# Performance work log

Measured on AMD Instinct MI355X. Metric: run time of the kernel, lower is better.

Reference implementation:

```python
import jax, jax.numpy as jnp
import numpy as np

B, Q, C, NH, NL, NP, DFF = 8, 300, 256, 8, 4, 4, 1024
DH = C // NH
SHAPES = [(100, 100), (50, 50), (25, 25), (13, 13)]  # (H, W) per level
LEN = sum(h * w for h, w in SHAPES)


def _ln(x, g, b):
    m = x.mean(-1, keepdims=True)
    v = ((x - m) ** 2).mean(-1, keepdims=True)
    return (x - m) / jnp.sqrt(v + 1e-5) * g + b


def _bilinear(v, loc, H, W):
    # v: [B, NH, H*W, DH]; loc: [B, NH, Q, NP, 2] normalized to [0,1]
    # grid_sample(align_corners=False, padding_mode='zeros') semantics
    x = loc[..., 0] * W - 0.5
    y = loc[..., 1] * H - 0.5
    x0 = jnp.floor(x)
    y0 = jnp.floor(y)
    dx = x - x0
    dy = y - y0
    out = jnp.zeros(x.shape + (v.shape[-1],), v.dtype)
    for xi, yi, wgt in ((x0, y0, (1 - dx) * (1 - dy)),
                        (x0 + 1, y0, dx * (1 - dy)),
                        (x0, y0 + 1, (1 - dx) * dy),
                        (x0 + 1, y0 + 1, dx * dy)):
        valid = ((xi >= 0) & (xi < W) & (yi >= 0) & (yi < H)).astype(v.dtype)
        idx = jnp.clip(yi, 0, H - 1).astype(jnp.int32) * W + jnp.clip(xi, 0, W - 1).astype(jnp.int32)
        g = jnp.take_along_axis(v, idx.reshape(idx.shape[0], idx.shape[1], -1)[..., None], axis=2)
        out = out + (wgt * valid)[..., None] * g.reshape(x.shape + (v.shape[-1],))
    return out


def _forward(tgt, reference_points, memory, query_pos_embed,
             Wq, bq, Wk, bk, Wv, bv, Wo, bo, g1, be1,
             W_off, b_off, W_attn, b_attn, W_val, b_val, W_out, b_out, g2, be2,
             W1, b1, W2, b2, g3, be3):
    scale = 1.0 / float(np.sqrt(DH))
    # ---- self attention (q = k = tgt + pos, v = tgt) ----
    qk = tgt + query_pos_embed
    q = (qk @ Wq + bq).reshape(B, Q, NH, DH)
    k = (qk @ Wk + bk).reshape(B, Q, NH, DH)
    v = (tgt @ Wv + bv).reshape(B, Q, NH, DH)
    attn = jax.nn.softmax(jnp.einsum('bqhd,bkhd->bhqk', q, k) * scale, axis=-1)
    sa = jnp.einsum('bhqk,bkhd->bqhd', attn, v).reshape(B, Q, C) @ Wo + bo
    t = _ln(tgt + sa, g1, be1)
    # ---- multi-scale deformable cross attention ----
    query = t + query_pos_embed
    value = (memory @ W_val + b_val).reshape(B, LEN, NH, DH).transpose(0, 2, 1, 3)  # [B,NH,LEN,DH]
    off = (query @ W_off + b_off).reshape(B, Q, NH, NL, NP, 2)
    aw = jax.nn.softmax((query @ W_attn + b_attn).reshape(B, Q, NH, NL * NP), axis=-1)
    aw = aw.reshape(B, Q, NH, NL, NP)
    wh = jnp.array([[w, h] for h, w in SHAPES], jnp.float32)  # offset normalizer (W, H)
    loc = reference_points[:, :, None, :, None, :] + off / wh[None, None, None, :, None, :]
    out = jnp.zeros((B, NH, Q, DH), t.dtype)
    start = 0
    for l, (h, w) in enumerate(SHAPES):
        v_l = value[:, :, start:start + h * w]
        loc_l = loc[:, :, :, l].transpose(0, 2, 1, 3, 4)  # [B,NH,Q,NP,2]
        samp = _bilinear(v_l, loc_l, h, w)                # [B,NH,Q,NP,DH]
        out = out + (samp * aw[:, :, :, l].transpose(0, 2, 1, 3)[..., None]).sum(3)
        start += h * w
    ca = out.transpose(0, 2, 1, 3).reshape(B, Q, C) @ W_out + b_out
    t = _ln(t + ca, g2, be2)
    # ---- FFN ----
    ff = jax.nn.relu(t @ W1 + b1) @ W2 + b2
    return _ln(t + ff, g3, be3)


def setup_inputs() -> dict:
    ks = jax.random.split(jax.random.key(0), 16)
    z, o = jnp.zeros, jnp.ones
    w = lambda i, sh: jax.random.normal(ks[i], sh, jnp.float32) * 0.02
    return {
        'tgt': jax.random.normal(ks[0], (B, Q, C), jnp.float32),
        'reference_points': jax.random.uniform(ks[1], (B, Q, NL, 2), jnp.float32),
        'memory': jax.random.normal(ks[2], (B, LEN, C), jnp.float32),
        'query_pos_embed': jax.random.normal(ks[3], (B, Q, C), jnp.float32),
        'Wq': w(4, (C, C)), 'bq': z(C), 'Wk': w(5, (C, C)), 'bk': z(C),
        'Wv': w(6, (C, C)), 'bv': z(C), 'Wo': w(7, (C, C)), 'bo': z(C),
        'g1': o(C), 'be1': z(C),
        'W_off': w(8, (C, NH * NL * NP * 2)), 'b_off': z(NH * NL * NP * 2),
        'W_attn': w(9, (C, NH * NL * NP)), 'b_attn': z(NH * NL * NP),
        'W_val': w(10, (C, C)), 'b_val': z(C), 'W_out': w(11, (C, C)), 'b_out': z(C),
        'g2': o(C), 'be2': z(C),
        'W1': w(12, (C, DFF)), 'b1': z(DFF), 'W2': w(13, (DFF, C)), 'b2': z(C),
        'g3': o(C), 'be3': z(C),
        'spatial_shapes': jnp.array(SHAPES, jnp.int32),
        'level_start_index': jnp.array(np.cumsum([0] + [h * w for h, w in SHAPES[:-1]]), jnp.int32),
    }


def reference(tgt, reference_points, memory, query_pos_embed,
              Wq, bq, Wk, bk, Wv, bv, Wo, bo, g1, be1,
              W_off, b_off, W_attn, b_attn, W_val, b_val, W_out, b_out, g2, be2,
              W1, b1, W2, b2, g3, be3, spatial_shapes, level_start_index):
    return _forward(tgt, reference_points, memory, query_pos_embed,
                    Wq, bq, Wk, bk, Wv, bv, Wo, bo, g1, be1,
                    W_off, b_off, W_attn, b_attn, W_val, b_val, W_out, b_out, g2, be2,
                    W1, b1, W2, b2, g3, be3)
```

## Files before the change

### kernel.cpp

```cpp
#include <hip/hip_runtime.h>
#include <hip/hip_bf16.h>
#include <math.h>

#define B_   8
#define Q_   300
#define C_   256
#define NH_  8
#define NL_  4
#define NP_  4
#define DFF_ 1024
#define DH_  32
#define LEN_ 13294
#define MQ_  (B_*Q_)
#define MV_  (B_*LEN_)
#define NSTRIP_ 3324

typedef __attribute__((ext_vector_type(4))) float f32x4;
typedef __attribute__((ext_vector_type(8))) short bf16x8;
typedef __hip_bfloat16 bf16;

#define GLOAD16(gp, lp) __builtin_amdgcn_global_load_lds( \
    (const __attribute__((address_space(1))) unsigned int*)(gp), \
    (__attribute__((address_space(3))) unsigned int*)(lp), 16, 0, 0)

__device__ __forceinline__ short f2bfbits(float x) {
    bf16 h = __float2bfloat16(x);
    return *reinterpret_cast<short*>(&h);
}


__device__ __forceinline__ void gmm64_body(char* smemraw, int bx, int by,
        const bf16* __restrict__ A, const bf16* __restrict__ Bt,
        const float* __restrict__ bias0, const float* __restrict__ bias1, int nsplit,
        float* __restrict__ outf, bf16* __restrict__ outh,
        int M, int N, int K, int RELU, int OUT_MODE) {
    bf16* As = (bf16*)smemraw;
    bf16* Bs = (bf16*)(smemraw + 4096);
    const int tid  = threadIdx.x;
    const int wid  = tid >> 6, lane = tid & 63;
    const int m0 = by * 64, n0 = bx * 64;
    const int wr = wid >> 1, wc = wid & 1;
    const int fr = lane & 15, fq = lane >> 4;
    const int rloc = wid * 16 + (lane >> 2);
    const int kof  = (lane & 3) * 8;
    f32x4 acc[2][2] = {};
    for (int k0 = 0; k0 < K; k0 += 32) {
        if (k0) __syncthreads();
        int gr = m0 + rloc; if (gr > M - 1) gr = M - 1;
        GLOAD16(A + (size_t)gr * K + k0 + kof, As + rloc * 32);
        int gc = n0 + rloc; if (gc > N - 1) gc = N - 1;
        GLOAD16(Bt + (size_t)gc * K + k0 + kof, Bs + rloc * 32);
        __syncthreads();
        bf16x8 af[2], bfr[2];
#pragma unroll
        for (int m = 0; m < 2; ++m)
            af[m] = *(const bf16x8*)(As + (wr * 32 + m * 16 + fr) * 32 + fq * 8);
#pragma unroll
        for (int n = 0; n < 2; ++n)
            bfr[n] = *(const bf16x8*)(Bs + (wc * 32 + n * 16 + fr) * 32 + fq * 8);
#pragma unroll
        for (int m = 0; m < 2; ++m)
#pragma unroll
            for (int n = 0; n < 2; ++n)
                acc[m][n] = __builtin_amdgcn_mfma_f32_16x16x32_bf16(af[m], bfr[n], acc[m][n], 0, 0, 0);
    }
#pragma unroll
    for (int m = 0; m < 2; ++m) {
#pragma unroll
        for (int n = 0; n < 2; ++n) {
            const int c = n0 + wc * 32 + n * 16 + fr;
            const float bs = (c < nsplit) ? bias0[c] : bias1[c - nsplit];
#pragma unroll
            for (int j = 0; j < 4; ++j) {
                const int r = m0 + wr * 32 + m * 16 + fq * 4 + j;
                if (r >= M) continue;
                float v = acc[m][n][j] + bs;
                if (RELU) v = fmaxf(v, 0.f);
                if (OUT_MODE == 0) outf[(size_t)r * N + c] = v;
                else               outh[(size_t)r * N + c] = __float2bfloat16(v);
            }
        }
    }
}

__device__ __forceinline__ void gmmV_body(char* smemraw, int bid,
        const float* __restrict__ A, const bf16* __restrict__ Bt,
        const float* __restrict__ bias, bf16* __restrict__ outh, int M) {
    short (*As)[8192] = (short(*)[8192])smemraw;
    const int tid = threadIdx.x;
    const int w = tid >> 6, lane = tid & 63;
    const int fr = lane & 15, fq = lane >> 4;
    const int r   = tid >> 3;
    const int itc = tid & 7;

    bf16x8 bc[4][8];
#pragma unroll
    for (int n = 0; n < 4; ++n)
#pragma unroll
        for (int it = 0; it < 8; ++it)
            bc[n][it] = *(const bf16x8*)(Bt + (size_t)(w * 64 + n * 16 + fr) * 256 + it * 32 + fq * 8);
    float bs[4];
#pragma unroll
    for (int n = 0; n < 4; ++n) bs[n] = bias[w * 64 + n * 16 + fr];

    const int sbase = bid * 4;
    float4 pf[8];

#define LOADA(s_) { \
        int row_ = (s_) * 32 + r; if (row_ > M - 1) row_ = M - 1; \
        const float4* p_ = (const float4*)(A + (size_t)row_ * 256 + itc * 32); \
        pf[0] = p_[0]; pf[1] = p_[1]; pf[2] = p_[2]; pf[3] = p_[3]; \
        pf[4] = p_[4]; pf[5] = p_[5]; pf[6] = p_[6]; pf[7] = p_[7]; }
#define WRITEA(buf_) { \
        short* dst_ = &As[buf_][itc * 1024 + r * 32]; \
        _Pragma("unroll") \
        for (int g_ = 0; g_ < 4; ++g_) { \
            float4 a0_ = pf[2 * g_], a1_ = pf[2 * g_ + 1]; \
            union { short h[8]; bf16x8 v; } cv_; \
            cv_.h[0] = f2bfbits(a0_.x); cv_.h[1] = f2bfbits(a0_.y); \
            cv_.h[2] = f2bfbits(a0_.z); cv_.h[3] = f2bfbits(a0_.w); \
            cv_.h[4] = f2bfbits(a1_.x); cv_.h[5] = f2bfbits(a1_.y); \
            cv_.h[6] = f2bfbits(a1_.z); cv_.h[7] = f2bfbits(a1_.w); \
            *(bf16x8*)(dst_ + g_ * 8) = cv_.v; \
        } }

    LOADA(sbase);
    WRITEA(0);
    __syncthreads();
    int buf = 0;
#pragma unroll 1
    for (int i = 0; i < 4; ++i) {
        const int s = sbase + i;
        if (s >= NSTRIP_) break;
        const bool more = (i < 3) && (s + 1 < NSTRIP_);
        if (more) LOADA(s + 1);
        f32x4 acc[2][4] = {};
#pragma unroll
        for (int it = 0; it < 8; ++it) {
            bf16x8 af[2];
#pragma unroll
            for (int m = 0; m < 2; ++m)
                af[m] = *(const bf16x8*)&As[buf][it * 1024 + (m * 16 + fr) * 32 + fq * 8];
#pragma unroll
            for (int m = 0; m < 2; ++m)
#pragma unroll
                for (int n = 0; n < 4; ++n)
                    acc[m][n] = __builtin_amdgcn_mfma_f32_16x16x32_bf16(af[m], bc[n][it], acc[m][n], 0, 0, 0);
        }
        if (more) WRITEA(buf ^ 1);
#pragma unroll
        for (int m = 0; m < 2; ++m)
#pragma unroll
            for (int n = 0; n < 4; ++n) {
                const int c = w * 64 + n * 16 + fr;
#pragma unroll
                for (int j = 0; j < 4; ++j) {
                    const int row = s * 32 + m * 16 + fq * 4 + j;
                    if (row < M)
                        outh[(size_t)row * 256 + c] = __float2bfloat16(acc[m][n][j] + bs[n]);
                }
            }
        if (more) __syncthreads();
        buf ^= 1;
    }
#undef LOADA
#undef WRITEA
}


__global__ __launch_bounds__(256) void k_prep(
        const float* __restrict__ Wq, const float* __restrict__ Wk,
        const float* __restrict__ Wv, const float* __restrict__ Wo,
        const float* __restrict__ Wval, const float* __restrict__ Woff,
        const float* __restrict__ Wattn, const float* __restrict__ Wout,
        const float* __restrict__ W1, const float* __restrict__ W2,
        bf16* __restrict__ Wqk_t, bf16* __restrict__ Wv_t, bf16* __restrict__ Wo_t,
        bf16* __restrict__ Wval_t, bf16* __restrict__ Woa_t, bf16* __restrict__ Wout_t,
        bf16* __restrict__ W1_t, bf16* __restrict__ W2_t,
        const float* __restrict__ tgt, const float* __restrict__ qpe,
        bf16* __restrict__ qk_o, bf16* __restrict__ tgt_o) {
    __shared__ float t[32][33];
    const int id = blockIdx.x;
    if (id < 992) {
        const float* W; bf16* D; int K, N, r;
        if      (id < 64)  { W = Wq;    D = Wqk_t;          K = 256;  N = 256;  r = id; }
        else if (id < 128) { W = Wk;    D = Wqk_t + 65536;  K = 256;  N = 256;  r = id - 64; }
        else if (id < 192) { W = Wv;    D = Wv_t;           K = 256;  N = 256;  r = id - 128; }
        else if (id < 256) { W = Wo;    D = Wo_t;           K = 256;  N = 256;  r = id - 192; }
        else if (id < 320) { W = Wval;  D = Wval_t;         K = 256;  N = 256;  r = id - 256; }
        else if (id < 384) { W = Woff;  D = Woa_t;          K = 256;  N = 256;  r = id - 320; }
        else if (id < 416) { W = Wattn; D = Woa_t + 65536;  K = 256;  N = 128;  r = id - 384; }
        else if (id < 480) { W = Wout;  D = Wout_t;         K = 256;  N = 256;  r = id - 416; }
        else if (id < 736) { W = W1;    D = W1_t;           K = 256;  N = 1024; r = id - 480; }
        else               { W = W2;    D = W2_t;           K = 1024; N = 256;  r = id - 736; }
        const int nx = N >> 5;
        const int k0 = (r / nx) * 32, n0 = (r % nx) * 32;
        const int c = threadIdx.x & 31, rr = threadIdx.x >> 5;
#pragma unroll
        for (int i = 0; i < 4; ++i)
            t[rr + i * 8][c] = W[(size_t)(k0 + rr + i * 8) * N + n0 + c];
        __syncthreads();
#pragma unroll
        for (int i = 0; i < 4; ++i)
            D[(size_t)(n0 + rr + i * 8) * K + k0 + c] = __float2bfloat16(t[c][rr + i * 8]);
    } else {
        const int i = (id - 992) * 256 + threadIdx.x;
        if (i >= MQ_ * C_ / 8) return;
        const float4* pa = (const float4*)(tgt + (size_t)i * 8);
        const float4* pb = (const float4*)(qpe + (size_t)i * 8);
        float4 x = pa[0], y = pa[1], u = pb[0], w = pb[1];
        union { bf16 h[8]; uint4 v; } s, tt;
        s.h[0] = __float2bfloat16(x.x + u.x); s.h[1] = __float2bfloat16(x.y + u.y);
        s.h[2] = __float2bfloat16(x.z + u.z); s.h[3] = __float2bfloat16(x.w + u.w);
        s.h[4] = __float2bfloat16(y.x + w.x); s.h[5] = __float2bfloat16(y.y + w.y);
        s.h[6] = __float2bfloat16(y.z + w.z); s.h[7] = __float2bfloat16(y.w + w.w);
        tt.h[0] = __float2bfloat16(x.x); tt.h[1] = __float2bfloat16(x.y);
        tt.h[2] = __float2bfloat16(x.z); tt.h[3] = __float2bfloat16(x.w);
        tt.h[4] = __float2bfloat16(y.x); tt.h[5] = __float2bfloat16(y.y);
        tt.h[6] = __float2bfloat16(y.z); tt.h[7] = __float2bfloat16(y.w);
        *(uint4*)(qk_o + (size_t)i * 8)  = s.v;
        *(uint4*)(tgt_o + (size_t)i * 8) = tt.v;
    }
}

__global__ __launch_bounds__(256, 2) void k_mega(
        const float* __restrict__ memory, const bf16* __restrict__ Wval_t,
        const float* __restrict__ b_val, bf16* __restrict__ value_bf,
        const bf16* __restrict__ qk_bf, const bf16* __restrict__ Wqk_t,
        const float* __restrict__ bq_, const float* __restrict__ bk_, bf16* __restrict__ qkbuf,
        const bf16* __restrict__ tgt_bf, const bf16* __restrict__ Wv_t,
        const float* __restrict__ bv_, bf16* __restrict__ vb) {
    __shared__ char smem[32768];
    const int bid = blockIdx.x;
    if (bid < 832) {
        gmmV_body(smem, bid, memory, Wval_t, b_val, value_bf, MV_);
    } else if (bid < 1136) {
        const int r = bid - 832;
        gmm64_body(smem, r & 7, r >> 3, qk_bf, Wqk_t, bq_, bk_, 256, nullptr, qkbuf, MQ_, 512, C_, 0, 1);
    } else {
        const int r = bid - 1136;
        gmm64_body(smem, r & 3, r >> 2, tgt_bf, Wv_t, bv_, bv_, 256, nullptr, vb, MQ_, 256, C_, 0, 1);
    }
}

template<int RELU, int OUT_MODE>
__global__ __launch_bounds__(256) void k_gmm64(const bf16* __restrict__ A,
                                               const bf16* __restrict__ Bt,
                                               const float* __restrict__ bias0,
                                               const float* __restrict__ bias1,
                                               int nsplit,
                                               float* __restrict__ outf,
                                               bf16* __restrict__ outh,
                                               int M, int N, int K) {
    __shared__ char smem[8192];
    gmm64_body(smem, blockIdx.x, blockIdx.y, A, Bt, bias0, bias1, nsplit,
               outf, outh, M, N, K, RELU, OUT_MODE);
}

__global__ __launch_bounds__(256) void k_attn(const bf16* __restrict__ qk2,
                                              const bf16* __restrict__ vb,
                                              bf16* __restrict__ sa) {
    __shared__ short Ks[304][40];
    __shared__ short Vt[32][328];
    __shared__ short Ps[4][16][168];
    const int tid = threadIdx.x, w = tid >> 6, lane = tid & 63;
    const int fr = lane & 15, fq = lane >> 4;
    const int bh = blockIdx.y, b = bh >> 3, h = bh & 7;
    const int qbase = blockIdx.x * 64;

    for (int k0 = 0; k0 < 300; k0 += 64) {
        int key = k0 + (tid >> 2);
        int dc = (tid & 3) * 8;
        if (key < 300) {
            *(bf16x8*)&Ks[key][dc] =
                *(const bf16x8*)&qk2[((size_t)(b * 300 + key)) * 512 + 256 + h * 32 + dc];
            bf16x8 v8 = *(const bf16x8*)&vb[((size_t)(b * 300 + key)) * 256 + h * 32 + dc];
#pragma unroll
            for (int i = 0; i < 8; ++i) Vt[dc + i][key] = v8[i];
        }
    }
    for (int i = tid; i < 32 * 20; i += 256) Vt[i & 31][300 + (i >> 5)] = 0;

    int qrow = qbase + w * 16 + fr;
    int qr = qrow < 300 ? qrow : 299;
    bf16x8 qf = *(const bf16x8*)&qk2[((size_t)(b * 300 + qr)) * 512 + h * 32 + fq * 8];
    __syncthreads();

    f32x4 s[19];
#pragma unroll
    for (int kf = 0; kf < 19; ++kf) {
        bf16x8 kfr = *(const bf16x8*)&Ks[kf * 16 + fr][fq * 8];
        f32x4 z = {};
        s[kf] = __builtin_amdgcn_mfma_f32_16x16x32_bf16(qf, kfr, z, 0, 0, 0);
    }
    const float scale = 0.17677669529663687f;
#pragma unroll
    for (int kf = 0; kf < 19; ++kf)
#pragma unroll
        for (int j = 0; j < 4; ++j) s[kf][j] *= scale;
    if (288 + fr >= 300) {
#pragma unroll
        for (int j = 0; j < 4; ++j) s[18][j] = -1e30f;
    }
    float mx[4], sm[4], inv[4];
#pragma unroll
    for (int j = 0; j < 4; ++j) {
        mx[j] = s[0][j];
#pragma unroll
        for (int kf = 1; kf < 19; ++kf) mx[j] = fmaxf(mx[j], s[kf][j]);
    }
#pragma unroll
    for (int off = 1; off < 16; off <<= 1)
#pragma unroll
        for (int j = 0; j < 4; ++j) mx[j] = fmaxf(mx[j], __shfl_xor(mx[j], off));
#pragma unroll
    for (int j = 0; j < 4; ++j) sm[j] = 0.f;
#pragma unroll
    for (int kf = 0; kf < 19; ++kf)
#pragma unroll
        for (int j = 0; j < 4; ++j) { s[kf][j] = expf(s[kf][j] - mx[j]); sm[j] += s[kf][j]; }
#pragma unroll
    for (int off = 1; off < 16; off <<= 1)
#pragma unroll
        for (int j = 0; j < 4; ++j) sm[j] += __shfl_xor(sm[j], off);
#pragma unroll
    for (int j = 0; j < 4; ++j) inv[j] = 1.f / sm[j];

    f32x4 o[2] = {};
#pragma unroll
    for (int half = 0; half < 2; ++half) {
        const int kfbeg = half * 10, kfend = half ? 19 : 10;
#pragma unroll
        for (int kf = kfbeg; kf < kfend; ++kf) {
            int gcol = kf * 16 + fr, lcol = gcol - half * 160;
            bool valid = gcol < 300;
#pragma unroll
            for (int j = 0; j < 4; ++j)
                Ps[w][fq * 4 + j][lcol] = valid ? f2bfbits(s[kf][j] * inv[j]) : (short)0;
        }
        if (half) {
            int r = lane >> 2, c0 = 144 + (lane & 3) * 4;
#pragma unroll
            for (int i = 0; i < 4; ++i) Ps[w][r][c0 + i] = 0;
        }
#pragma unroll
        for (int ks = 0; ks < 5; ++ks) {
            bf16x8 pa = *(const bf16x8*)&Ps[w][fr][ks * 32 + fq * 8];
#pragma unroll
            for (int n = 0; n < 2; ++n) {
                bf16x8 vf = *(const bf16x8*)&Vt[n * 16 + fr][half * 160 + ks * 32 + fq * 8];
                o[n] = __builtin_amdgcn_mfma_f32_16x16x32_bf16(pa, vf, o[n], 0, 0, 0);
            }
        }
    }
#pragma unroll
    for (int n = 0; n < 2; ++n)
#pragma unroll
        for (int j = 0; j < 4; ++j) {
            int row = qbase + w * 16 + fq * 4 + j;
            if (row < 300)
                sa[((size_t)(b * 300 + row)) * 256 + h * 32 + n * 16 + fr] = __float2bfloat16(o[n][j]);
        }
}

template<int WB>
__global__ __launch_bounds__(256) void k_ln(const float* __restrict__ x,
                                            const float* __restrict__ res,
                                            const float* __restrict__ qpe,
                                            const float* __restrict__ g,
                                            const float* __restrict__ be,
                                            float* __restrict__ out,
                                            bf16* __restrict__ outh, int rows) {
    const int row = blockIdx.x;
    const int tid = threadIdx.x;
    float v = x[row * C_ + tid] + res[row * C_ + tid];
    __shared__ float red[4];
    float s = v;
#pragma unroll
    for (int off = 32; off; off >>= 1) s += __shfl_xor(s, off);
    if ((tid & 63) == 0) red[tid >> 6] = s;
    __syncthreads();
    float mean = (red[0] + red[1] + red[2] + red[3]) * (1.f / C_);
    float dv = v - mean;
    float s2 = dv * dv;
    __syncthreads();
#pragma unroll
    for (int off = 32; off; off >>= 1) s2 += __shfl_xor(s2, off);
    if ((tid & 63) == 0) red[tid >> 6] = s2;
    __syncthreads();
    float var = (red[0] + red[1] + red[2] + red[3]) * (1.f / C_);
    float rstd = 1.f / sqrtf(var + 1e-5f);
    float y = dv * rstd * g[tid] + be[tid];
    out[row * C_ + tid] = y;
    if (WB == 1) outh[row * C_ + tid] = __float2bfloat16(y);
    if (WB == 2) outh[row * C_ + tid] = __float2bfloat16(y + qpe[row * C_ + tid]);
}

__global__ __launch_bounds__(256) void k_sample(const bf16* __restrict__ value,
                                                const float* __restrict__ refp,
                                                const float* __restrict__ offaw,
                                                bf16* __restrict__ out) {
    const int t  = blockIdx.x * 256 + threadIdx.x;
    const int d2 = t & 15;
    const int g  = t >> 4;
    const int h  = g & 7;
    const int bq = g >> 3;
    const int b  = bq / Q_;
    const int starts[4] = {0, 10000, 12500, 13125};
    const int HW[4]     = {100, 50, 25, 13};
    const float* offp = offaw + (size_t)bq * 384 + h * 32;

    float myl = offaw[(size_t)bq * 384 + 256 + h * 16 + d2];
    float mxl = myl;
#pragma unroll
    for (int o = 1; o < 16; o <<= 1) mxl = fmaxf(mxl, __shfl_xor(mxl, o));
    float e = expf(myl - mxl);
    float se = e;
#pragma unroll
    for (int o = 1; o < 16; o <<= 1) se += __shfl_xor(se, o);
    const float myaw = e / se;

    float acc0 = 0.f, acc1 = 0.f;
#pragma unroll
    for (int l = 0; l < NL_; ++l) {
        const int Hl = HW[l], Wl = HW[l], st = starts[l];
        const float rx = refp[(bq * NL_ + l) * 2 + 0];
        const float ry = refp[(bq * NL_ + l) * 2 + 1];
        const bf16* vbase = value + ((size_t)b * LEN_ + st) * C_ + h * DH_ + d2 * 2;
#pragma unroll
        for (int p = 0; p < NP_; ++p) {
            const float ox = offp[l * 8 + p * 2 + 0];
            const float oy = offp[l * 8 + p * 2 + 1];
            const float x = (rx + ox / (float)Wl) * (float)Wl - 0.5f;
            const float y = (ry + oy / (float)Hl) * (float)Hl - 0.5f;
            const float x0 = floorf(x), y0 = floorf(y);
            const float dx = x - x0, dy = y - y0;
            const int ix0 = (int)x0, iy0 = (int)y0;
            const float aw = __shfl(myaw, l * 4 + p, 16);
            float s0 = 0.f, s1 = 0.f;
#pragma unroll
            for (int cor = 0; cor < 4; ++cor) {
                const int xi = ix0 + (cor & 1), yi = iy0 + (cor >> 1);
                if (xi >= 0 && xi < Wl && yi >= 0 && yi < Hl) {
                    const float wg = (cor & 1 ? dx : 1.f - dx) * (cor >> 1 ? dy : 1.f - dy);
                    const unsigned u = *(const unsigned*)(vbase + (size_t)(yi * Wl + xi) * C_);
                    bf16 lo, hi;
                    *reinterpret_cast<short*>(&lo) = (short)(u & 0xFFFF);
                    *reinterpret_cast<short*>(&hi) = (short)(u >> 16);
                    s0 += wg * __bfloat162float(lo);
                    s1 += wg * __bfloat162float(hi);
                }
            }
            acc0 += aw * s0;
            acc1 += aw * s1;
        }
    }
    union { short h2[2]; unsigned u; } pack;
    pack.h2[0] = f2bfbits(acc0);
    pack.h2[1] = f2bfbits(acc1);
    *(unsigned*)(out + (size_t)bq * C_ + h * DH_ + d2 * 2) = pack.u;
}

extern "C" void kernel_launch(void* const* d_in, const int* in_sizes, int n_in,
                              void* d_out, int out_size, void* d_ws, size_t ws_size,
                              hipStream_t stream) {
    const float* tgt    = (const float*)d_in[0];
    const float* refp   = (const float*)d_in[1];
    const float* memory = (const float*)d_in[2];
    const float* qpe    = (const float*)d_in[3];
    const float* Wq     = (const float*)d_in[4];  const float* bq_  = (const float*)d_in[5];
    const float* Wk     = (const float*)d_in[6];  const float* bk_  = (const float*)d_in[7];
    const float* Wv     = (const float*)d_in[8];  const float* bv_  = (const float*)d_in[9];
    const float* Wo     = (const float*)d_in[10]; const float* bo_  = (const float*)d_in[11];
    const float* g1     = (const float*)d_in[12]; const float* be1  = (const float*)d_in[13];
    const float* W_off  = (const float*)d_in[14]; const float* b_off  = (const float*)d_in[15];
    const float* W_attn = (const float*)d_in[16]; const float* b_attn = (const float*)d_in[17];
    const float* W_val  = (const float*)d_in[18]; const float* b_val  = (const float*)d_in[19];
    const float* W_out  = (const float*)d_in[20]; const float* b_out  = (const float*)d_in[21];
    const float* g2     = (const float*)d_in[22]; const float* be2  = (const float*)d_in[23];
    const float* W1     = (const float*)d_in[24]; const float* b1   = (const float*)d_in[25];
    const float* W2     = (const float*)d_in[26]; const float* b2   = (const float*)d_in[27];
    const float* g3     = (const float*)d_in[28]; const float* be3  = (const float*)d_in[29];
    float* out = (float*)d_out;

    char* base = (char*)d_ws;
    size_t off = 0;
    auto alloc = [&](size_t bytes) -> char* {
        char* p = base + off; off = (off + bytes + 255) & ~(size_t)255; return p;
    };
    float* t1       = (float*)alloc(MQ_ * C_ * 4);
    float* offaw    = (float*)alloc((size_t)MQ_ * 384 * 4);
    bf16*  query_bf = (bf16*) alloc(MQ_ * C_ * 2);
    bf16*  dsout_bf = (bf16*) alloc(MQ_ * C_ * 2);
    bf16*  Wqk_t  = (bf16*)alloc(512 * C_ * 2);
    bf16*  Wv_t   = (bf16*)alloc(C_ * C_ * 2);
    bf16*  Wo_t   = (bf16*)alloc(C_ * C_ * 2);
    bf16*  Wval_t = (bf16*)alloc(C_ * C_ * 2);
    bf16*  Woa_t  = (bf16*)alloc(384 * C_ * 2);
    bf16*  Wout_t = (bf16*)alloc(C_ * C_ * 2);
    bf16*  W1_t   = (bf16*)alloc(C_ * DFF_ * 2);
    bf16*  W2_t   = (bf16*)alloc(DFF_ * C_ * 2);
    bf16*  value_bf = (bf16*)alloc((size_t)MV_ * C_ * 2);
    char*  U      = alloc((size_t)MV_ * C_ * 2);
    bf16*  qk_bf  = (bf16*)(U);
    bf16*  tgt_bf = (bf16*)(U + 1228800);
    bf16*  qkbuf  = (bf16*)(U + 2457600);
    bf16*  vb     = (bf16*)(U + 4915200);
    bf16*  sa_bf  = (bf16*)(U + 6144000);
    float* saO    = (float*)(U + 7372800);
    float* ca     = (float*)(U);
    float* t2     = (float*)(U + 2457600);
    bf16*  t2_bf  = (bf16*) (U + 4915200);
    bf16*  ff1_bf = (bf16*) (U + 6144000);
    float* ff2    = (float*)(U + 11059200);

    k_prep<<<1292, 256, 0, stream>>>(Wq, Wk, Wv, Wo, W_val, W_off, W_attn, W_out, W1, W2,
                                     Wqk_t, Wv_t, Wo_t, Wval_t, Woa_t, Wout_t, W1_t, W2_t,
                                     tgt, qpe, qk_bf, tgt_bf);
    k_mega<<<1288, 256, 0, stream>>>(memory, Wval_t, b_val, value_bf,
                                     qk_bf, Wqk_t, bq_, bk_, qkbuf,
                                     tgt_bf, Wv_t, bv_, vb);
    k_attn<<<dim3(5, 64), 256, 0, stream>>>(qkbuf, vb, sa_bf);
    k_gmm64<0,0><<<dim3(4, 38), 256, 0, stream>>>(sa_bf, Wo_t, bo_, bo_, 256, saO, nullptr, MQ_, 256, C_);
    k_ln<2><<<2400, 256, 0, stream>>>(tgt, saO, qpe, g1, be1, t1, query_bf, MQ_);
    k_gmm64<0,0><<<dim3(6, 38), 256, 0, stream>>>(query_bf, Woa_t, b_off, b_attn, 256, offaw, nullptr, MQ_, 384, C_);
    k_sample<<<1200, 256, 0, stream>>>(value_bf, refp, offaw, dsout_bf);
    k_gmm64<0,0><<<dim3(4, 38), 256, 0, stream>>>(dsout_bf, Wout_t, b_out, b_out, 256, ca, nullptr, MQ_, 256, C_);
    k_ln<1><<<2400, 256, 0, stream>>>(t1, ca, nullptr, g2, be2, t2, t2_bf, MQ_);
    k_gmm64<1,1><<<dim3(16, 38), 256, 0, stream>>>(t2_bf, W1_t, b1, b1, DFF_, nullptr, ff1_bf, MQ_, DFF_, C_);
    k_gmm64<0,0><<<dim3(4, 38), 256, 0, stream>>>(ff1_bf, W2_t, b2, b2, 256, ff2, nullptr, MQ_, C_, DFF_);
    k_ln<0><<<2400, 256, 0, stream>>>(t2, ff2, nullptr, g3, be3, out, nullptr, MQ_);
}
```

Before: 151.4 us.

## Fuse output-projection GEMMs with residual add and LayerNorm into one kernel

Replaces each of the three GEMM plus separate LayerNorm kernel pairs with a single kernel. Each block computes a full 64x256 row tile so the residual add, bias and LayerNorm run in registers using cross-lane shuffles. This removes three launches and the fp32 round trip of the intermediate GEMM output. The trade-off is that each GEMM now runs on only 38 blocks instead of 152, with 16 accumulators per wave, which lowers parallelism on a GPU with many compute units. The workspace layout is also rearranged because the old aliased buffers are no longer needed.

```diff
diff --git a/kernel.cpp b/kernel.cpp
--- a/kernel.cpp
+++ b/kernel.cpp
@@ -257,6 +257,79 @@
                outf, outh, M, N, K, RELU, OUT_MODE);
 }
 
+template<int WB>
+__global__ __launch_bounds__(256) void k_gemmln(
+        const bf16* __restrict__ A, const bf16* __restrict__ Bt,
+        const float* __restrict__ bias,
+        const float* __restrict__ res, const float* __restrict__ qpe,
+        const float* __restrict__ g, const float* __restrict__ be,
+        float* __restrict__ outf, bf16* __restrict__ outh,
+        int M, int K) {
+    __shared__ bf16 As[64 * 32];
+    __shared__ bf16 Bs[256 * 32];
+    const int tid = threadIdx.x, w = tid >> 6, lane = tid & 63;
+    const int fr = lane & 15, fq = lane >> 4;
+    const int m0 = blockIdx.x * 64;
+    const int ar = tid >> 2;
+    const int kof = (tid & 3) * 8;
+    const int br = tid >> 2;
+    f32x4 acc[16] = {};
+    for (int k0 = 0; k0 < K; k0 += 32) {
+        if (k0) __syncthreads();
+        int gr = m0 + ar; if (gr > M - 1) gr = M - 1;
+        GLOAD16(A + (size_t)gr * K + k0 + kof, As + ar * 32);
+#pragma unroll
+        for (int s = 0; s < 4; ++s)
+            GLOAD16(Bt + (size_t)(s * 64 + br) * K + k0 + kof, Bs + (s * 64 + br) * 32);
+        __syncthreads();
+        bf16x8 af = *(const bf16x8*)(As + (w * 16 + fr) * 32 + fq * 8);
+#pragma unroll
+        for (int n = 0; n < 16; ++n) {
+            bf16x8 bfr = *(const bf16x8*)(Bs + (n * 16 + fr) * 32 + fq * 8);
+            acc[n] = __builtin_amdgcn_mfma_f32_16x16x32_bf16(af, bfr, acc[n], 0, 0, 0);
+        }
+    }
+    float bsv[16], gv[16], bev[16];
+#pragma unroll
+    for (int n = 0; n < 16; ++n) {
+        bsv[n] = bias[n * 16 + fr];
+        gv[n]  = g[n * 16 + fr];
+        bev[n] = be[n * 16 + fr];
+    }
+#pragma unroll
+    for (int j = 0; j < 4; ++j) {
+        const int row = m0 + w * 16 + fq * 4 + j;
+        const int rowc = row < M ? row : M - 1;
+        const float* rr = res + (size_t)rowc * 256 + fr;
+        float s = 0.f;
+#pragma unroll
+        for (int n = 0; n < 16; ++n) {
+            acc[n][j] += bsv[n] + rr[n * 16];
+            s += acc[n][j];
+        }
+#pragma unroll
+        for (int o = 1; o < 16; o <<= 1) s += __shfl_xor(s, o);
+        const float mean = s * (1.f / 256.f);
+        float s2 = 0.f;
+#pragma unroll
+        for (int n = 0; n < 16; ++n) { float d = acc[n][j] - mean; s2 += d * d; }
+#pragma unroll
+        for (int o = 1; o < 16; o <<= 1) s2 += __shfl_xor(s2, o);
+        const float rstd = 1.f / sqrtf(s2 * (1.f / 256.f) + 1e-5f);
+        if (row < M) {
+#pragma unroll
+            for (int n = 0; n < 16; ++n) {
+                const int c = n * 16 + fr;
+                const float y = (acc[n][j] - mean) * rstd * gv[n] + bev[n];
+                outf[(size_t)row * 256 + c] = y;
+                if (WB == 1) outh[(size_t)row * 256 + c] = __float2bfloat16(y);
+                if (WB == 2) outh[(size_t)row * 256 + c] =
+                    __float2bfloat16(y + qpe[(size_t)row * 256 + c]);
+            }
+        }
+    }
+}
+
 __global__ __launch_bounds__(256) void k_attn(const bf16* __restrict__ qk2,
                                               const bf16* __restrict__ vb,
                                               bf16* __restrict__ sa) {
@@ -361,39 +434,6 @@
             if (row < 300)
                 sa[((size_t)(b * 300 + row)) * 256 + h * 32 + n * 16 + fr] = __float2bfloat16(o[n][j]);
         }
-}
-
-template<int WB>
-__global__ __launch_bounds__(256) void k_ln(const float* __restrict__ x,
-                                            const float* __restrict__ res,
-                                            const float* __restrict__ qpe,
-                                            const float* __restrict__ g,
-                                            const float* __restrict__ be,
-                                            float* __restrict__ out,
-                                            bf16* __restrict__ outh, int rows) {
-    const int row = blockIdx.x;
-    const int tid = threadIdx.x;
-    float v = x[row * C_ + tid] + res[row * C_ + tid];
-    __shared__ float red[4];
-    float s = v;
-#pragma unroll
-    for (int off = 32; off; off >>= 1) s += __shfl_xor(s, off);
-    if ((tid & 63) == 0) red[tid >> 6] = s;
-    __syncthreads();
-    float mean = (red[0] + red[1] + red[2] + red[3]) * (1.f / C_);
-    float dv = v - mean;
-    float s2 = dv * dv;
-    __syncthreads();
-#pragma unroll
-    for (int off = 32; off; off >>= 1) s2 += __shfl_xor(s2, off);
-    if ((tid & 63) == 0) red[tid >> 6] = s2;
-    __syncthreads();
-    float var = (red[0] + red[1] + red[2] + red[3]) * (1.f / C_);
-    float rstd = 1.f / sqrtf(var + 1e-5f);
-    float y = dv * rstd * g[tid] + be[tid];
-    out[row * C_ + tid] = y;
-    if (WB == 1) outh[row * C_ + tid] = __float2bfloat16(y);
-    if (WB == 2) outh[row * C_ + tid] = __float2bfloat16(y + qpe[row * C_ + tid]);
 }
 
 __global__ __launch_bounds__(256) void k_sample(const bf16* __restrict__ value,
@@ -489,9 +529,12 @@
         char* p = base + off; off = (off + bytes + 255) & ~(size_t)255; return p;
     };
     float* t1       = (float*)alloc(MQ_ * C_ * 4);
+    float* t2       = (float*)alloc(MQ_ * C_ * 4);
     float* offaw    = (float*)alloc((size_t)MQ_ * 384 * 4);
     bf16*  query_bf = (bf16*) alloc(MQ_ * C_ * 2);
     bf16*  dsout_bf = (bf16*) alloc(MQ_ * C_ * 2);
+    bf16*  t2_bf    = (bf16*) alloc(MQ_ * C_ * 2);
+    bf16*  ff1_bf   = (bf16*) alloc((size_t)MQ_ * DFF_ * 2);
     bf16*  Wqk_t  = (bf16*)alloc(512 * C_ * 2);
     bf16*  Wv_t   = (bf16*)alloc(C_ * C_ * 2);
     bf16*  Wo_t   = (bf16*)alloc(C_ * C_ * 2);
@@ -501,18 +544,12 @@
     bf16*  W1_t   = (bf16*)alloc(C_ * DFF_ * 2);
     bf16*  W2_t   = (bf16*)alloc(DFF_ * C_ * 2);
     bf16*  value_bf = (bf16*)alloc((size_t)MV_ * C_ * 2);
-    char*  U      = alloc((size_t)MV_ * C_ * 2);
+    char*  U      = alloc(9830400);
     bf16*  qk_bf  = (bf16*)(U);
     bf16*  tgt_bf = (bf16*)(U + 1228800);
     bf16*  qkbuf  = (bf16*)(U + 2457600);
     bf16*  vb     = (bf16*)(U + 4915200);
     bf16*  sa_bf  = (bf16*)(U + 6144000);
-    float* saO    = (float*)(U + 7372800);
-    float* ca     = (float*)(U);
-    float* t2     = (float*)(U + 2457600);
-    bf16*  t2_bf  = (bf16*) (U + 4915200);
-    bf16*  ff1_bf = (bf16*) (U + 6144000);
-    float* ff2    = (float*)(U + 11059200);
 
     k_prep<<<1292, 256, 0, stream>>>(Wq, Wk, Wv, Wo, W_val, W_off, W_attn, W_out, W1, W2,
                                      Wqk_t, Wv_t, Wo_t, Wval_t, Woa_t, Wout_t, W1_t, W2_t,
@@ -521,13 +558,13 @@
                                      qk_bf, Wqk_t, bq_, bk_, qkbuf,
                                      tgt_bf, Wv_t, bv_, vb);
     k_attn<<<dim3(5, 64), 256, 0, stream>>>(qkbuf, vb, sa_bf);
-    k_gmm64<0,0><<<dim3(4, 38), 256, 0, stream>>>(sa_bf, Wo_t, bo_, bo_, 256, saO, nullptr, MQ_, 256, C_);
-    k_ln<2><<<2400, 256, 0, stream>>>(tgt, saO, qpe, g1, be1, t1, query_bf, MQ_);
+    k_gemmln<2><<<38, 256, 0, stream>>>(sa_bf, Wo_t, bo_, tgt, qpe, g1, be1,
+                                        t1, query_bf, MQ_, C_);
     k_gmm64<0,0><<<dim3(6, 38), 256, 0, stream>>>(query_bf, Woa_t, b_off, b_attn, 256, offaw, nullptr, MQ_, 384, C_);
     k_sample<<<1200, 256, 0, stream>>>(value_bf, refp, offaw, dsout_bf);
-    k_gmm64<0,0><<<dim3(4, 38), 256, 0, stream>>>(dsout_bf, Wout_t, b_out, b_out, 256, ca, nullptr, MQ_, 256, C_);
-    k_ln<1><<<2400, 256, 0, stream>>>(t1, ca, nullptr, g2, be2, t2, t2_bf, MQ_);
+    k_gemmln<1><<<38, 256, 0, stream>>>(dsout_bf, Wout_t, b_out, t1, nullptr, g2, be2,
+                                        t2, t2_bf, MQ_, C_);
     k_gmm64<1,1><<<dim3(16, 38), 256, 0, stream>>>(t2_bf, W1_t, b1, b1, DFF_, nullptr, ff1_bf, MQ_, DFF_, C_);
-    k_gmm64<0,0><<<dim3(4, 38), 256, 0, stream>>>(ff1_bf, W2_t, b2, b2, 256, ff2, nullptr, MQ_, C_, DFF_);
-    k_ln<0><<<2400, 256, 0, stream>>>(t2, ff2, nullptr, g3, be3, out, nullptr, MQ_);
-}
+    k_gemmln<0><<<38, 256, 0, stream>>>(ff1_bf, W2_t, b2, t2, nullptr, g3, be3,
+                                        out, nullptr, MQ_, DFF_);
+}
```

Result: slower. 168.2 us (+11.1%).
